# Performance work log

Measured on AMD Instinct MI355X. Metric: run time of the kernel, lower is better.

## Reference

```python
import jax, jax.numpy as jnp
import numpy as np

IN_DIM, HID, B, T = 128, 512, 32, 2048
TAU_X, TAU = 200.0, 5


def setup_inputs() -> dict:
    key = jax.random.key(0)
    ks = jax.random.split(key, 12)
    s = 0.05
    return {
        "in_seq": jax.random.normal(ks[0], (B, T, IN_DIM), jnp.float32),
        "We1": jax.random.normal(ks[1], (IN_DIM, HID), jnp.float32) * s,
        "be1": jnp.zeros((HID,), jnp.float32),
        "We2": jax.random.normal(ks[2], (HID, HID), jnp.float32) * s,
        "be2": jnp.zeros((HID,), jnp.float32),
        "We3": jax.random.normal(ks[3], (HID, HID), jnp.float32) * s,
        "be3": jnp.zeros((HID,), jnp.float32),
        # decoder: Linear+tanh, Linear+tanh
        "Wd1": jax.random.normal(ks[4], (HID, HID), jnp.float32) * s,
        "bd1": jnp.zeros((HID,), jnp.float32),
        "Wd2": jax.random.normal(ks[5], (HID, IN_DIM), jnp.float32) * s,
        "bd2": jnp.zeros((IN_DIM,), jnp.float32),
        # recurrent weight (torch: randn * 0.1)
        "W": jax.random.normal(ks[6], (HID, HID), jnp.float32) * 0.1,
    }


def reference(in_seq, We1, be1, We2, be2, We3, be3, Wd1, bd1, Wd2, bd2, W):
    def encoder(u):
        h = jnp.tanh(u @ We1 + be1)
        h = jnp.tanh(h @ We2 + be2)
        return jnp.tanh(h @ We3 + be3)

    def decoder(h):
        h = jnp.tanh(h @ Wd1 + bd1)
        return jnp.tanh(h @ Wd2 + bd2)

    x_seq = encoder(in_seq)  # [B, T, H]
    Tlen = in_seq.shape[1]
    # teacher forcing flag per step: t % tau == 0 and t > 0
    t_idx = jnp.arange(Tlen)
    tf_flags = (t_idx % TAU == 0) & (t_idx > 0)

    xs_T = jnp.swapaxes(x_seq, 0, 1)  # [T, B, H]

    def step(x, inp):
        flag, xs_t = inp
        x = jnp.where(flag, xs_t, x)
        dx = -x + jnp.tanh(x) @ W.T
        x = x + dx / TAU_X
        return x, decoder(x)  # per-step prediction [B, in_dim]

    x0 = x_seq[:, 0, :]
    _, preds = jax.lax.scan(step, x0, (tf_flags, xs_T))  # preds: [T, B, in_dim]
    x_pred = jnp.swapaxes(preds, 0, 1)  # [B, T, in_dim]
    x_recon = decoder(x_seq)  # [B, T, in_dim]
    return (x_pred, x_recon)
```

## Files before the change

### kernel.cpp

```cpp
#include <hip/hip_runtime.h>
#include <stdint.h>

#define B_SZ  32
#define T_SZ  2048
#define IN_D  128
#define HID   512
#define NCHAIN 410
#define MREC  (NCHAIN * B_SZ)
#define INV_TAUX 0.005f

typedef __attribute__((ext_vector_type(8))) short bf16x8;
typedef __attribute__((ext_vector_type(4))) float f32x4;
typedef __attribute__((ext_vector_type(4))) float float4v;
typedef __attribute__((ext_vector_type(4))) unsigned short u16x4;
typedef __attribute__((ext_vector_type(8))) unsigned short u16x8;

#define MFMA(b, a, c) __builtin_amdgcn_mfma_f32_16x16x32_bf16((b), (a), (c), 0, 0, 0)

__device__ __forceinline__ unsigned short f2bf(float x) {
  union { float f; unsigned int u; } v; v.f = x;
  unsigned int r = v.u + 0x7FFFu + ((v.u >> 16) & 1u);
  return (unsigned short)(r >> 16);
}
__device__ __forceinline__ float bf2f(unsigned short b) {
  union { unsigned int u; float f; } v; v.u = ((unsigned int)b) << 16;
  return v.f;
}
__device__ __forceinline__ float fast_tanh(float x) {
  float ax = fabsf(x);
  float e = __expf(-2.0f * ax);
  float r = (1.0f - e) * __builtin_amdgcn_rcpf(1.0f + e);
  return x < 0.0f ? -r : r;
}
__device__ __forceinline__ void gload_lds16(const void* g, void* l) {
  __builtin_amdgcn_global_load_lds(
      reinterpret_cast<__attribute__((address_space(1))) void*>(reinterpret_cast<uintptr_t>(g)),
      reinterpret_cast<__attribute__((address_space(3))) void*>(reinterpret_cast<uintptr_t>(l)),
      16, 0, 0);
}


__global__ __launch_bounds__(512) void enc_fused_k(
    const float* __restrict__ in_seq,
    const unsigned short* __restrict__ wt,
    const float* __restrict__ be1, const float* __restrict__ be2,
    const float* __restrict__ be3,
    unsigned short* __restrict__ xseq)
{
  __shared__ __attribute__((aligned(16))) unsigned short sH[64 * 512];
  unsigned short* sA = sH;

  const int tid = threadIdx.x;
  const int m0 = blockIdx.x * 64;
  const int wave = tid >> 6, lane = tid & 63;
  const int wn = wave;
  const int lrow = lane & 15, lhi = lane >> 4, sw = lrow & 7;

#pragma unroll
  for (int p = 0; p < 2; ++p) {
    int id = (p << 9) + tid;
    int row = id >> 4, cc = id & 15;
    const float* src = in_seq + (size_t)(m0 + row) * IN_D + (cc << 3);
    float4v u0 = *(const float4v*)src;
    float4v u1 = *(const float4v*)(src + 4);
    u16x8 h;
    h[0] = f2bf(u0[0]); h[1] = f2bf(u0[1]); h[2] = f2bf(u0[2]); h[3] = f2bf(u0[3]);
    h[4] = f2bf(u1[0]); h[5] = f2bf(u1[1]); h[6] = f2bf(u1[2]); h[7] = f2bf(u1[3]);
    int slot = (cc & 8) | ((cc & 7) ^ (row & 7));
    *(u16x8*)(sA + (row << 7) + (slot << 3)) = h;
  }
  __syncthreads();

  f32x4 acc[4][4];
  const unsigned short* Bts[3] = {wt, wt + 65536, wt + 327680};
  const float* bss[3] = {be1, be2, be3};

  for (int l = 0; l < 3; ++l) {
    const unsigned short* lsrc = sH;
    const int lstr = (l == 0) ? 128 : 512;
    const int nk = (l == 0) ? 4 : 16;
    const unsigned short* bl = Bts[l] + (lane << 3);
    const int nfb = (wn << 2) * nk;
    const float* bias = bss[l];

#pragma unroll
    for (int m = 0; m < 4; ++m)
#pragma unroll
      for (int n = 0; n < 4; ++n) acc[m][n] = (f32x4){0.f, 0.f, 0.f, 0.f};

    bf16x8 b0[4], b1[4];
#pragma unroll
    for (int n = 0; n < 4; ++n)
      b0[n] = *(const bf16x8*)(bl + ((nfb + n * nk) << 9));

    for (int kk = 0; kk < nk; kk += 2) {
#pragma unroll
      for (int n = 0; n < 4; ++n)
        b1[n] = *(const bf16x8*)(bl + ((nfb + n * nk + kk + 1) << 9));
      {
        const int c = (kk << 2) + lhi;
        const int slot = (c & ~7) | ((c & 7) ^ sw);
        bf16x8 af[4];
#pragma unroll
        for (int m = 0; m < 4; ++m)
          af[m] = *(const bf16x8*)(lsrc + (m * 16 + lrow) * lstr + (slot << 3));
#pragma unroll
        for (int n = 0; n < 4; ++n)
#pragma unroll
          for (int m = 0; m < 4; ++m)
            acc[m][n] = MFMA(b0[n], af[m], acc[m][n]);
      }
      if (kk + 2 < nk) {
#pragma unroll
        for (int n = 0; n < 4; ++n)
          b0[n] = *(const bf16x8*)(bl + ((nfb + n * nk + kk + 2) << 9));
      }
      {
        const int c = ((kk + 1) << 2) + lhi;
        const int slot = (c & ~7) | ((c & 7) ^ sw);
        bf16x8 af[4];
#pragma unroll
        for (int m = 0; m < 4; ++m)
          af[m] = *(const bf16x8*)(lsrc + (m * 16 + lrow) * lstr + (slot << 3));
#pragma unroll
        for (int n = 0; n < 4; ++n)
#pragma unroll
          for (int m = 0; m < 4; ++m)
            acc[m][n] = MFMA(b1[n], af[m], acc[m][n]);
      }
    }
    __syncthreads();
#pragma unroll
    for (int n = 0; n < 4; ++n) {
      const int col0 = (wn << 6) + n * 16 + (lhi << 2);
      const float4v bv = *(const float4v*)(bias + col0);
      const int c2 = col0 >> 3;
#pragma unroll
      for (int m = 0; m < 4; ++m) {
        const int row = m * 16 + lrow;
        const int slot2 = (c2 & ~7) | ((c2 & 7) ^ (row & 7));
        u16x4 h;
#pragma unroll
        for (int q = 0; q < 4; ++q) h[q] = f2bf(fast_tanh(acc[m][n][q] + bv[q]));
        *(u16x4*)(sH + (row << 9) + (slot2 << 3) + (col0 & 7)) = h;
      }
    }
    __syncthreads();
  }

#pragma unroll
  for (int p = 0; p < 8; ++p) {
    int id = (p << 9) + tid;
    int row = id >> 6, cc = id & 63;
    int slot = (cc & ~7) | ((cc & 7) ^ (row & 7));
    u16x8 v = *(const u16x8*)(sH + (row << 9) + (slot << 3));
    *(u16x8*)(xseq + ((size_t)(m0 + row) << 9) + (cc << 3)) = v;
  }
}

__global__ __launch_bounds__(512) void dec_fused_k(
    const unsigned short* __restrict__ X,
    const unsigned short* __restrict__ Wd1t,
    const unsigned short* __restrict__ Wd2t,
    const float* __restrict__ bd1, const float* __restrict__ bd2,
    float* __restrict__ out)
{
  __shared__ __attribute__((aligned(16))) unsigned short sH[64 * 512];
  unsigned short* sX = sH;

  const int tid = threadIdx.x;
  const int m0 = blockIdx.x * 64;
  const int wave = tid >> 6, lane = tid & 63;
  const int wn = wave;
  const int lrow = lane & 15, lhi = lane >> 4, sw = lrow & 7;

  char* lX = (char*)sX + tid * 16;
#pragma unroll
  for (int p = 0; p < 8; ++p) {
    int id = (p << 9) + tid;
    int row = id >> 6, cc = id & 63;
    int gcc = (cc & ~7) | ((cc & 7) ^ (row & 7));
    gload_lds16(X + ((size_t)(m0 + row) << 9) + (gcc << 3), lX + (p << 13));
  }
  __syncthreads();

  f32x4 acc[4][4];
#pragma unroll
  for (int m = 0; m < 4; ++m)
#pragma unroll
    for (int n = 0; n < 4; ++n) acc[m][n] = (f32x4){0.f, 0.f, 0.f, 0.f};

  {
    const unsigned short* bl = Wd1t + (lane << 3);
    const int nfb = (wn << 2) << 4;
    bf16x8 b0[4], b1[4];
#pragma unroll
    for (int n = 0; n < 4; ++n)
      b0[n] = *(const bf16x8*)(bl + ((nfb + (n << 4)) << 9));
    for (int kk = 0; kk < 16; kk += 2) {
#pragma unroll
      for (int n = 0; n < 4; ++n)
        b1[n] = *(const bf16x8*)(bl + ((nfb + (n << 4) + kk + 1) << 9));
      {
        const int c = (kk << 2) + lhi;
        const int slot = (c & ~7) | ((c & 7) ^ sw);
        bf16x8 af[4];
#pragma unroll
        for (int m = 0; m < 4; ++m)
          af[m] = *(const bf16x8*)(sX + ((m * 16 + lrow) << 9) + (slot << 3));
#pragma unroll
        for (int n = 0; n < 4; ++n)
#pragma unroll
          for (int m = 0; m < 4; ++m)
            acc[m][n] = MFMA(b0[n], af[m], acc[m][n]);
      }
      if (kk + 2 < 16) {
#pragma unroll
        for (int n = 0; n < 4; ++n)
          b0[n] = *(const bf16x8*)(bl + ((nfb + (n << 4) + kk + 2) << 9));
      }
      {
        const int c = ((kk + 1) << 2) + lhi;
        const int slot = (c & ~7) | ((c & 7) ^ sw);
        bf16x8 af[4];
#pragma unroll
        for (int m = 0; m < 4; ++m)
          af[m] = *(const bf16x8*)(sX + ((m * 16 + lrow) << 9) + (slot << 3));
#pragma unroll
        for (int n = 0; n < 4; ++n)
#pragma unroll
          for (int m = 0; m < 4; ++m)
            acc[m][n] = MFMA(b1[n], af[m], acc[m][n]);
      }
    }
  }
  __syncthreads();
#pragma unroll
  for (int n = 0; n < 4; ++n) {
    const int col0 = (wn << 6) + n * 16 + (lhi << 2);
    const float4v bv = *(const float4v*)(bd1 + col0);
    const int c2 = col0 >> 3;
#pragma unroll
    for (int m = 0; m < 4; ++m) {
      const int row = m * 16 + lrow;
      const int slot2 = (c2 & ~7) | ((c2 & 7) ^ (row & 7));
      u16x4 h;
#pragma unroll
      for (int q = 0; q < 4; ++q) h[q] = f2bf(fast_tanh(acc[m][n][q] + bv[q]));
      *(u16x4*)(sH + (row << 9) + (slot2 << 3) + (col0 & 7)) = h;
    }
  }
  __syncthreads();

  f32x4 acc2[4];
#pragma unroll
  for (int m = 0; m < 4; ++m) acc2[m] = (f32x4){0.f, 0.f, 0.f, 0.f};

  {
    const unsigned short* bl = Wd2t + (lane << 3);
    const int nfb = wn << 4;
    bf16x8 c0, c1;
    c0 = *(const bf16x8*)(bl + ((nfb + 0) << 9));
    for (int kk = 0; kk < 16; kk += 2) {
      c1 = *(const bf16x8*)(bl + ((nfb + kk + 1) << 9));
      {
        const int c = (kk << 2) + lhi;
        const int slot = (c & ~7) | ((c & 7) ^ sw);
#pragma unroll
        for (int m = 0; m < 4; ++m) {
          bf16x8 af = *(const bf16x8*)(sH + ((m * 16 + lrow) << 9) + (slot << 3));
          acc2[m] = MFMA(c0, af, acc2[m]);
        }
      }
      if (kk + 2 < 16)
        c0 = *(const bf16x8*)(bl + ((nfb + kk + 2) << 9));
      {
        const int c = ((kk + 1) << 2) + lhi;
        const int slot = (c & ~7) | ((c & 7) ^ sw);
#pragma unroll
        for (int m = 0; m < 4; ++m) {
          bf16x8 af = *(const bf16x8*)(sH + ((m * 16 + lrow) << 9) + (slot << 3));
          acc2[m] = MFMA(c1, af, acc2[m]);
        }
      }
    }
  }
  {
    const int col0 = (wn << 4) + (lhi << 2);
    const float4v bv = *(const float4v*)(bd2 + col0);
#pragma unroll
    for (int m = 0; m < 4; ++m) {
      const int row = m * 16 + lrow;
      float4v o;
#pragma unroll
      for (int q = 0; q < 4; ++q) o[q] = fast_tanh(acc2[m][q] + bv[q]);
      *(float4v*)(out + (size_t)(m0 + row) * IN_D + col0) = o;
    }
  }
}

__global__ __launch_bounds__(512) void rec2_k(
    const unsigned short* __restrict__ Wrec,
    const float* __restrict__ st_in,
    float* __restrict__ st_out,
    unsigned short* __restrict__ xsall,
    int s)
{
  __shared__ __attribute__((aligned(16))) unsigned short sA[32 * 512];

  const int tid = threadIdx.x;
  const int chain = blockIdx.x;
  const int wave = tid >> 6, lane = tid & 63;
  const int wn = wave;
  const int lrow = lane & 15, lhi = lane >> 4, sw = lrow & 7;
  const size_t rbase = (size_t)chain * 32;

#pragma unroll
  for (int p = 0; p < 4; ++p) {
    int id = (p << 9) + tid;
    int row = id >> 6, cc = id & 63;
    int gc = (cc & ~7) | ((cc & 7) ^ (row & 7));
    const float* src = st_in + (rbase + row) * HID + (gc << 3);
    float4v u0 = *(const float4v*)src;
    float4v u1 = *(const float4v*)(src + 4);
    u16x8 h;
    h[0] = f2bf(fast_tanh(u0[0])); h[1] = f2bf(fast_tanh(u0[1]));
    h[2] = f2bf(fast_tanh(u0[2])); h[3] = f2bf(fast_tanh(u0[3]));
    h[4] = f2bf(fast_tanh(u1[0])); h[5] = f2bf(fast_tanh(u1[1]));
    h[6] = f2bf(fast_tanh(u1[2])); h[7] = f2bf(fast_tanh(u1[3]));
    *(u16x8*)(sA + (row << 9) + (cc << 3)) = h;
  }
  __syncthreads();

  f32x4 acc[2][4];
#pragma unroll
  for (int m = 0; m < 2; ++m)
#pragma unroll
    for (int n = 0; n < 4; ++n) acc[m][n] = (f32x4){0.f, 0.f, 0.f, 0.f};

  const unsigned short* bl = Wrec + (lane << 3);
  const int nfb = (wn << 2) << 4;

  bf16x8 b0[4], b1[4];
#pragma unroll
  for (int n = 0; n < 4; ++n)
    b0[n] = *(const bf16x8*)(bl + ((nfb + (n << 4)) << 9));
  for (int kk = 0; kk < 16; kk += 2) {
#pragma unroll
    for (int n = 0; n < 4; ++n)
      b1[n] = *(const bf16x8*)(bl + ((nfb + (n << 4) + kk + 1) << 9));
    {
      const int c = (kk << 2) + lhi;
      const int slot = (c & ~7) | ((c & 7) ^ sw);
      bf16x8 af0 = *(const bf16x8*)(sA + (lrow << 9) + (slot << 3));
      bf16x8 af1 = *(const bf16x8*)(sA + ((16 + lrow) << 9) + (slot << 3));
#pragma unroll
      for (int n = 0; n < 4; ++n) {
        acc[0][n] = MFMA(b0[n], af0, acc[0][n]);
        acc[1][n] = MFMA(b0[n], af1, acc[1][n]);
      }
    }
    if (kk + 2 < 16) {
#pragma unroll
      for (int n = 0; n < 4; ++n)
        b0[n] = *(const bf16x8*)(bl + ((nfb + (n << 4) + kk + 2) << 9));
    }
    {
      const int c = ((kk + 1) << 2) + lhi;
      const int slot = (c & ~7) | ((c & 7) ^ sw);
      bf16x8 af0 = *(const bf16x8*)(sA + (lrow << 9) + (slot << 3));
      bf16x8 af1 = *(const bf16x8*)(sA + ((16 + lrow) << 9) + (slot << 3));
#pragma unroll
      for (int n = 0; n < 4; ++n) {
        acc[0][n] = MFMA(b1[n], af0, acc[0][n]);
        acc[1][n] = MFMA(b1[n], af1, acc[1][n]);
      }
    }
  }

  const int t = chain * 5 + s;
#pragma unroll
  for (int n = 0; n < 4; ++n) {
    const int col0 = (wn << 6) + n * 16 + (lhi << 2);
#pragma unroll
    for (int m = 0; m < 2; ++m) {
      const int row = m * 16 + lrow;
      const size_t gi = (rbase + row) * HID + col0;
      float4v x = *(const float4v*)(st_in + gi);
      float4v xn;
#pragma unroll
      for (int q = 0; q < 4; ++q) xn[q] = x[q] + (acc[m][n][q] - x[q]) * INV_TAUX;
      *(float4v*)(st_out + gi) = xn;
      if (t < T_SZ) {
        u16x4 h;
#pragma unroll
        for (int q = 0; q < 4; ++q) h[q] = f2bf(xn[q]);
        *(u16x4*)(xsall + ((size_t)row * T_SZ + t) * HID + col0) = h;
      }
    }
  }
}

__global__ void chain_init_k(const unsigned short* __restrict__ xseq,
                             float* __restrict__ st0) {
  int idx = blockIdx.x * blockDim.x + threadIdx.x;
  if (idx >= MREC * HID) return;
  int r = idx >> 9;
  int c = idx & 511;
  int chain = r >> 5;
  int b = r & 31;
  st0[idx] = bf2f(xseq[((size_t)b * T_SZ + chain * 5) * HID + c]);
}

__global__ void prep_k(const float* __restrict__ We1, const float* __restrict__ We2,
                       const float* __restrict__ We3, const float* __restrict__ Wd1,
                       const float* __restrict__ Wd2, const float* __restrict__ W,
                       unsigned short* __restrict__ wt) {
  int idx = blockIdx.x * blockDim.x + threadIdx.x;
  if (idx >= 1179648) return;
  unsigned short v;
  if (idx < 65536) {
    int i = idx, lane = (i >> 3) & 63, t2 = i >> 9;
    int kk = t2 & 3, nf = t2 >> 2;
    int n = (nf << 4) + (lane & 15), k = (kk << 5) + ((lane >> 4) << 3) + (i & 7);
    v = f2bf(We1[k * 512 + n]);
  } else if (idx < 327680) {
    int i = idx - 65536, lane = (i >> 3) & 63, t2 = i >> 9;
    int kk = t2 & 15, nf = t2 >> 4;
    int n = (nf << 4) + (lane & 15), k = (kk << 5) + ((lane >> 4) << 3) + (i & 7);
    v = f2bf(We2[k * 512 + n]);
  } else if (idx < 589824) {
    int i = idx - 327680, lane = (i >> 3) & 63, t2 = i >> 9;
    int kk = t2 & 15, nf = t2 >> 4;
    int n = (nf << 4) + (lane & 15), k = (kk << 5) + ((lane >> 4) << 3) + (i & 7);
    v = f2bf(We3[k * 512 + n]);
  } else if (idx < 851968) {
    int i = idx - 589824, lane = (i >> 3) & 63, t2 = i >> 9;
    int kk = t2 & 15, nf = t2 >> 4;
    int n = (nf << 4) + (lane & 15), k = (kk << 5) + ((lane >> 4) << 3) + (i & 7);
    v = f2bf(Wd1[k * 512 + n]);
  } else if (idx < 917504) {
    int i = idx - 851968, lane = (i >> 3) & 63, t2 = i >> 9;
    int kk = t2 & 15, nf = t2 >> 4;
    int n = (nf << 4) + (lane & 15), k = (kk << 5) + ((lane >> 4) << 3) + (i & 7);
    v = f2bf(Wd2[k * 128 + n]);
  } else {
    int i = idx - 917504, lane = (i >> 3) & 63, t2 = i >> 9;
    int kk = t2 & 15, nf = t2 >> 4;
    int n = (nf << 4) + (lane & 15), k = (kk << 5) + ((lane >> 4) << 3) + (i & 7);
    v = f2bf(W[(n << 9) + k]);
  }
  wt[idx] = v;
}

__global__ void sentinel_k(float* out, float v) { out[0] = v; }

extern "C" void kernel_launch(void* const* d_in, const int* in_sizes, int n_in,
                              void* d_out, int out_size, void* d_ws, size_t ws_size,
                              hipStream_t stream) {
  const float* in_seq = (const float*)d_in[0];
  const float* We1 = (const float*)d_in[1];
  const float* be1 = (const float*)d_in[2];
  const float* We2 = (const float*)d_in[3];
  const float* be2 = (const float*)d_in[4];
  const float* We3 = (const float*)d_in[5];
  const float* be3 = (const float*)d_in[6];
  const float* Wd1 = (const float*)d_in[7];
  const float* bd1 = (const float*)d_in[8];
  const float* Wd2 = (const float*)d_in[9];
  const float* bd2 = (const float*)d_in[10];
  const float* W   = (const float*)d_in[11];

  const int NROW = B_SZ * T_SZ;
  const size_t OFF_XSEQ = 0;
  const size_t OFF_WT   = (size_t)NROW * HID * 2;
  const size_t OFF_ST0  = OFF_WT + 2359296;
  const size_t OFF_ST1  = OFF_ST0 + (size_t)MREC * HID * 4;
  const size_t REQUIRED = OFF_ST1 + (size_t)MREC * HID * 4;

  float* outp = (float*)d_out;
  float* outr = outp + (size_t)NROW * IN_D;

  if (ws_size < REQUIRED) {
    sentinel_k<<<1, 1, 0, stream>>>(outp, (float)(ws_size >> 20));
    return;
  }

  char* ws = (char*)d_ws;
  unsigned short* xseq = (unsigned short*)(ws + OFF_XSEQ);
  unsigned short* wt   = (unsigned short*)(ws + OFF_WT);
  unsigned short* Wd1t = wt + 589824;
  unsigned short* Wd2t = wt + 851968;
  unsigned short* Wrec = wt + 917504;
  float* st0 = (float*)(ws + OFF_ST0);
  float* st1 = (float*)(ws + OFF_ST1);

  prep_k<<<4608, 256, 0, stream>>>(We1, We2, We3, Wd1, Wd2, W, wt);
  enc_fused_k<<<1024, 512, 0, stream>>>(in_seq, wt, be1, be2, be3, xseq);
  dec_fused_k<<<1024, 512, 0, stream>>>(xseq, Wd1t, Wd2t, bd1, bd2, outr);
  chain_init_k<<<(MREC * HID + 255) / 256, 256, 0, stream>>>(xseq, st0);
  for (int s = 0; s < 5; ++s) {
    const float* sIn  = (s & 1) ? st1 : st0;
    float*       sOut = (s & 1) ? st0 : st1;
    rec2_k<<<NCHAIN, 512, 0, stream>>>(Wrec, sIn, sOut, xseq, s);
  }
  dec_fused_k<<<1024, 512, 0, stream>>>(xseq, Wd1t, Wd2t, bd1, bd2, outp);
}
```

Before: 476.5 us.

## Fuse recon decoder into encoder and merge recurrence steps into one kernel

The encoder kernel now runs the two decoder layers directly on its LDS-resident tile, producing x_recon without re-reading x_seq from global memory. The five per-step recurrence launches and the chain-init kernel become one kernel that keeps the fp32 chain state in LDS across the five steps. This removes global state round-trips, the workspace for state buffers, and several launches. In exchange, the fused encoder kernel gets longer and the recurrence kernel uses much more LDS per block.

```diff
diff --git a/kernel.cpp b/kernel.cpp
--- a/kernel.cpp
+++ b/kernel.cpp
@@ -6,7 +6,6 @@
 #define IN_D  128
 #define HID   512
 #define NCHAIN 410
-#define MREC  (NCHAIN * B_SZ)
 #define INV_TAUX 0.005f
 
 typedef __attribute__((ext_vector_type(8))) short bf16x8;
@@ -40,12 +39,16 @@
 }
 
 
-__global__ __launch_bounds__(512) void enc_fused_k(
+__global__ __launch_bounds__(512) void enc5_k(
     const float* __restrict__ in_seq,
     const unsigned short* __restrict__ wt,
     const float* __restrict__ be1, const float* __restrict__ be2,
     const float* __restrict__ be3,
-    unsigned short* __restrict__ xseq)
+    const unsigned short* __restrict__ Wd1t,
+    const unsigned short* __restrict__ Wd2t,
+    const float* __restrict__ bd1, const float* __restrict__ bd2,
+    unsigned short* __restrict__ xseq,
+    float* __restrict__ outr)
 {
   __shared__ __attribute__((aligned(16))) unsigned short sH[64 * 512];
   unsigned short* sA = sH;
@@ -76,7 +79,6 @@
   const float* bss[3] = {be1, be2, be3};
 
   for (int l = 0; l < 3; ++l) {
-    const unsigned short* lsrc = sH;
     const int lstr = (l == 0) ? 128 : 512;
     const int nk = (l == 0) ? 4 : 16;
     const unsigned short* bl = Bts[l] + (lane << 3);
@@ -103,7 +105,7 @@
         bf16x8 af[4];
 #pragma unroll
         for (int m = 0; m < 4; ++m)
-          af[m] = *(const bf16x8*)(lsrc + (m * 16 + lrow) * lstr + (slot << 3));
+          af[m] = *(const bf16x8*)(sH + (m * 16 + lrow) * lstr + (slot << 3));
 #pragma unroll
         for (int n = 0; n < 4; ++n)
 #pragma unroll
@@ -121,7 +123,7 @@
         bf16x8 af[4];
 #pragma unroll
         for (int m = 0; m < 4; ++m)
-          af[m] = *(const bf16x8*)(lsrc + (m * 16 + lrow) * lstr + (slot << 3));
+          af[m] = *(const bf16x8*)(sH + (m * 16 + lrow) * lstr + (slot << 3));
 #pragma unroll
         for (int n = 0; n < 4; ++n)
 #pragma unroll
@@ -155,6 +157,119 @@
     int slot = (cc & ~7) | ((cc & 7) ^ (row & 7));
     u16x8 v = *(const u16x8*)(sH + (row << 9) + (slot << 3));
     *(u16x8*)(xseq + ((size_t)(m0 + row) << 9) + (cc << 3)) = v;
+  }
+
+#pragma unroll
+  for (int m = 0; m < 4; ++m)
+#pragma unroll
+    for (int n = 0; n < 4; ++n) acc[m][n] = (f32x4){0.f, 0.f, 0.f, 0.f};
+
+  {
+    const unsigned short* bl = Wd1t + (lane << 3);
+    const int nfb = (wn << 2) << 4;
+    bf16x8 b0[4], b1[4];
+#pragma unroll
+    for (int n = 0; n < 4; ++n)
+      b0[n] = *(const bf16x8*)(bl + ((nfb + (n << 4)) << 9));
+    for (int kk = 0; kk < 16; kk += 2) {
+#pragma unroll
+      for (int n = 0; n < 4; ++n)
+        b1[n] = *(const bf16x8*)(bl + ((nfb + (n << 4) + kk + 1) << 9));
+      {
+        const int c = (kk << 2) + lhi;
+        const int slot = (c & ~7) | ((c & 7) ^ sw);
+        bf16x8 af[4];
+#pragma unroll
+        for (int m = 0; m < 4; ++m)
+          af[m] = *(const bf16x8*)(sH + ((m * 16 + lrow) << 9) + (slot << 3));
+#pragma unroll
+        for (int n = 0; n < 4; ++n)
+#pragma unroll
+          for (int m = 0; m < 4; ++m)
+            acc[m][n] = MFMA(b0[n], af[m], acc[m][n]);
+      }
+      if (kk + 2 < 16) {
+#pragma unroll
+        for (int n = 0; n < 4; ++n)
+          b0[n] = *(const bf16x8*)(bl + ((nfb + (n << 4) + kk + 2) << 9));
+      }
+      {
+        const int c = ((kk + 1) << 2) + lhi;
+        const int slot = (c & ~7) | ((c & 7) ^ sw);
+        bf16x8 af[4];
+#pragma unroll
+        for (int m = 0; m < 4; ++m)
+          af[m] = *(const bf16x8*)(sH + ((m * 16 + lrow) << 9) + (slot << 3));
+#pragma unroll
+        for (int n = 0; n < 4; ++n)
+#pragma unroll
+          for (int m = 0; m < 4; ++m)
+            acc[m][n] = MFMA(b1[n], af[m], acc[m][n]);
+      }
+    }
+  }
+  __syncthreads();
+#pragma unroll
+  for (int n = 0; n < 4; ++n) {
+    const int col0 = (wn << 6) + n * 16 + (lhi << 2);
+    const float4v bv = *(const float4v*)(bd1 + col0);
+    const int c2 = col0 >> 3;
+#pragma unroll
+    for (int m = 0; m < 4; ++m) {
+      const int row = m * 16 + lrow;
+      const int slot2 = (c2 & ~7) | ((c2 & 7) ^ (row & 7));
+      u16x4 h;
+#pragma unroll
+      for (int q = 0; q < 4; ++q) h[q] = f2bf(fast_tanh(acc[m][n][q] + bv[q]));
+      *(u16x4*)(sH + (row << 9) + (slot2 << 3) + (col0 & 7)) = h;
+    }
+  }
+  __syncthreads();
+
+  f32x4 acc2[4];
+#pragma unroll
+  for (int m = 0; m < 4; ++m) acc2[m] = (f32x4){0.f, 0.f, 0.f, 0.f};
+
+  {
+    const unsigned short* bl = Wd2t + (lane << 3);
+    const int nfb = wn << 4;
+    bf16x8 c0, c1;
+    c0 = *(const bf16x8*)(bl + ((nfb + 0) << 9));
+    for (int kk = 0; kk < 16; kk += 2) {
+      c1 = *(const bf16x8*)(bl + ((nfb + kk + 1) << 9));
+      {
+        const int c = (kk << 2) + lhi;
+        const int slot = (c & ~7) | ((c & 7) ^ sw);
+#pragma unroll
+        for (int m = 0; m < 4; ++m) {
+          bf16x8 af = *(const bf16x8*)(sH + ((m * 16 + lrow) << 9) + (slot << 3));
+          acc2[m] = MFMA(c0, af, acc2[m]);
+        }
+      }
+      if (kk + 2 < 16)
+        c0 = *(const bf16x8*)(bl + ((nfb + kk + 2) << 9));
+      {
+        const int c = ((kk + 1) << 2) + lhi;
+        const int slot = (c & ~7) | ((c & 7) ^ sw);
+#pragma unroll
+        for (int m = 0; m < 4; ++m) {
+          bf16x8 af = *(const bf16x8*)(sH + ((m * 16 + lrow) << 9) + (slot << 3));
+          acc2[m] = MFMA(c1, af, acc2[m]);
+        }
+      }
+    }
+  }
+  {
+    const int col0 = (wn << 4) + (lhi << 2);
+    const float4v bv = *(const float4v*)(bd2 + col0);
+#pragma unroll
+    for (int m = 0; m < 4; ++m) {
+      const int row = m * 16 + lrow;
+      float4v o;
+#pragma unroll
+      for (int q = 0; q < 4; ++q) o[q] = fast_tanh(acc2[m][q] + bv[q]);
+      *(float4v*)(outr + (size_t)(m0 + row) * IN_D + col0) = o;
+    }
   }
 }
 
@@ -299,117 +414,117 @@
   }
 }
 
-__global__ __launch_bounds__(512) void rec2_k(
+__global__ __launch_bounds__(512) void rec_all_k(
     const unsigned short* __restrict__ Wrec,
-    const float* __restrict__ st_in,
-    float* __restrict__ st_out,
-    unsigned short* __restrict__ xsall,
-    int s)
+    unsigned short* __restrict__ xsall)
 {
+  __shared__ float xst[32][516];
   __shared__ __attribute__((aligned(16))) unsigned short sA[32 * 512];
 
   const int tid = threadIdx.x;
   const int chain = blockIdx.x;
+  const int t0 = chain * 5;
   const int wave = tid >> 6, lane = tid & 63;
   const int wn = wave;
   const int lrow = lane & 15, lhi = lane >> 4, sw = lrow & 7;
-  const size_t rbase = (size_t)chain * 32;
 
 #pragma unroll
   for (int p = 0; p < 4; ++p) {
     int id = (p << 9) + tid;
-    int row = id >> 6, cc = id & 63;
-    int gc = (cc & ~7) | ((cc & 7) ^ (row & 7));
-    const float* src = st_in + (rbase + row) * HID + (gc << 3);
-    float4v u0 = *(const float4v*)src;
-    float4v u1 = *(const float4v*)(src + 4);
-    u16x8 h;
-    h[0] = f2bf(fast_tanh(u0[0])); h[1] = f2bf(fast_tanh(u0[1]));
-    h[2] = f2bf(fast_tanh(u0[2])); h[3] = f2bf(fast_tanh(u0[3]));
-    h[4] = f2bf(fast_tanh(u1[0])); h[5] = f2bf(fast_tanh(u1[1]));
-    h[6] = f2bf(fast_tanh(u1[2])); h[7] = f2bf(fast_tanh(u1[3]));
-    *(u16x8*)(sA + (row << 9) + (cc << 3)) = h;
+    int row = id >> 6, c8 = (id & 63) << 3;
+    u16x8 v = *(const u16x8*)(xsall + (((size_t)row * T_SZ + t0) << 9) + c8);
+#pragma unroll
+    for (int e = 0; e < 8; ++e) xst[row][c8 + e] = bf2f(v[e]);
   }
   __syncthreads();
-
-  f32x4 acc[2][4];
-#pragma unroll
-  for (int m = 0; m < 2; ++m)
-#pragma unroll
-    for (int n = 0; n < 4; ++n) acc[m][n] = (f32x4){0.f, 0.f, 0.f, 0.f};
 
   const unsigned short* bl = Wrec + (lane << 3);
   const int nfb = (wn << 2) << 4;
 
-  bf16x8 b0[4], b1[4];
-#pragma unroll
-  for (int n = 0; n < 4; ++n)
-    b0[n] = *(const bf16x8*)(bl + ((nfb + (n << 4)) << 9));
-  for (int kk = 0; kk < 16; kk += 2) {
+  for (int s = 0; s < 5; ++s) {
+#pragma unroll
+    for (int p = 0; p < 4; ++p) {
+      int id = (p << 9) + tid;
+      int row = id >> 6, cc = id & 63;
+      int gc = (cc & ~7) | ((cc & 7) ^ (row & 7));
+      const float* src = &xst[row][gc << 3];
+      float4v u0 = *(const float4v*)src;
+      float4v u1 = *(const float4v*)(src + 4);
+      u16x8 h;
+      h[0] = f2bf(fast_tanh(u0[0])); h[1] = f2bf(fast_tanh(u0[1]));
+      h[2] = f2bf(fast_tanh(u0[2])); h[3] = f2bf(fast_tanh(u0[3]));
+      h[4] = f2bf(fast_tanh(u1[0])); h[5] = f2bf(fast_tanh(u1[1]));
+      h[6] = f2bf(fast_tanh(u1[2])); h[7] = f2bf(fast_tanh(u1[3]));
+      *(u16x8*)(sA + (row << 9) + (cc << 3)) = h;
+    }
+    __syncthreads();
+
+    f32x4 acc[2][4];
+#pragma unroll
+    for (int m = 0; m < 2; ++m)
+#pragma unroll
+      for (int n = 0; n < 4; ++n) acc[m][n] = (f32x4){0.f, 0.f, 0.f, 0.f};
+
+    bf16x8 b0[4], b1[4];
 #pragma unroll
     for (int n = 0; n < 4; ++n)
-      b1[n] = *(const bf16x8*)(bl + ((nfb + (n << 4) + kk + 1) << 9));
-    {
-      const int c = (kk << 2) + lhi;
-      const int slot = (c & ~7) | ((c & 7) ^ sw);
-      bf16x8 af0 = *(const bf16x8*)(sA + (lrow << 9) + (slot << 3));
-      bf16x8 af1 = *(const bf16x8*)(sA + ((16 + lrow) << 9) + (slot << 3));
-#pragma unroll
-      for (int n = 0; n < 4; ++n) {
-        acc[0][n] = MFMA(b0[n], af0, acc[0][n]);
-        acc[1][n] = MFMA(b0[n], af1, acc[1][n]);
-      }
-    }
-    if (kk + 2 < 16) {
+      b0[n] = *(const bf16x8*)(bl + ((nfb + (n << 4)) << 9));
+    for (int kk = 0; kk < 16; kk += 2) {
 #pragma unroll
       for (int n = 0; n < 4; ++n)
-        b0[n] = *(const bf16x8*)(bl + ((nfb + (n << 4) + kk + 2) << 9));
-    }
-    {
-      const int c = ((kk + 1) << 2) + lhi;
-      const int slot = (c & ~7) | ((c & 7) ^ sw);
-      bf16x8 af0 = *(const bf16x8*)(sA + (lrow << 9) + (slot << 3));
-      bf16x8 af1 = *(const bf16x8*)(sA + ((16 + lrow) << 9) + (slot << 3));
-#pragma unroll
-      for (int n = 0; n < 4; ++n) {
-        acc[0][n] = MFMA(b1[n], af0, acc[0][n]);
-        acc[1][n] = MFMA(b1[n], af1, acc[1][n]);
-      }
-    }
-  }
-
-  const int t = chain * 5 + s;
-#pragma unroll
-  for (int n = 0; n < 4; ++n) {
-    const int col0 = (wn << 6) + n * 16 + (lhi << 2);
-#pragma unroll
-    for (int m = 0; m < 2; ++m) {
-      const int row = m * 16 + lrow;
-      const size_t gi = (rbase + row) * HID + col0;
-      float4v x = *(const float4v*)(st_in + gi);
-      float4v xn;
-#pragma unroll
-      for (int q = 0; q < 4; ++q) xn[q] = x[q] + (acc[m][n][q] - x[q]) * INV_TAUX;
-      *(float4v*)(st_out + gi) = xn;
-      if (t < T_SZ) {
-        u16x4 h;
-#pragma unroll
-        for (int q = 0; q < 4; ++q) h[q] = f2bf(xn[q]);
-        *(u16x4*)(xsall + ((size_t)row * T_SZ + t) * HID + col0) = h;
-      }
-    }
-  }
-}
-
-__global__ void chain_init_k(const unsigned short* __restrict__ xseq,
-                             float* __restrict__ st0) {
-  int idx = blockIdx.x * blockDim.x + threadIdx.x;
-  if (idx >= MREC * HID) return;
-  int r = idx >> 9;
-  int c = idx & 511;
-  int chain = r >> 5;
-  int b = r & 31;
-  st0[idx] = bf2f(xseq[((size_t)b * T_SZ + chain * 5) * HID + c]);
+        b1[n] = *(const bf16x8*)(bl + ((nfb + (n << 4) + kk + 1) << 9));
+      {
+        const int c = (kk << 2) + lhi;
+        const int slot = (c & ~7) | ((c & 7) ^ sw);
+        bf16x8 af0 = *(const bf16x8*)(sA + (lrow << 9) + (slot << 3));
+        bf16x8 af1 = *(const bf16x8*)(sA + ((16 + lrow) << 9) + (slot << 3));
+#pragma unroll
+        for (int n = 0; n < 4; ++n) {
+          acc[0][n] = MFMA(b0[n], af0, acc[0][n]);
+          acc[1][n] = MFMA(b0[n], af1, acc[1][n]);
+        }
+      }
+      if (kk + 2 < 16) {
+#pragma unroll
+        for (int n = 0; n < 4; ++n)
+          b0[n] = *(const bf16x8*)(bl + ((nfb + (n << 4) + kk + 2) << 9));
+      }
+      {
+        const int c = ((kk + 1) << 2) + lhi;
+        const int slot = (c & ~7) | ((c & 7) ^ sw);
+        bf16x8 af0 = *(const bf16x8*)(sA + (lrow << 9) + (slot << 3));
+        bf16x8 af1 = *(const bf16x8*)(sA + ((16 + lrow) << 9) + (slot << 3));
+#pragma unroll
+        for (int n = 0; n < 4; ++n) {
+          acc[0][n] = MFMA(b1[n], af0, acc[0][n]);
+          acc[1][n] = MFMA(b1[n], af1, acc[1][n]);
+        }
+      }
+    }
+    __syncthreads();
+
+    const int t = t0 + s;
+#pragma unroll
+    for (int n = 0; n < 4; ++n) {
+      const int col0 = (wn << 6) + n * 16 + (lhi << 2);
+#pragma unroll
+      for (int m = 0; m < 2; ++m) {
+        const int row = m * 16 + lrow;
+        float4v x = *(const float4v*)(&xst[row][col0]);
+        float4v xn;
+#pragma unroll
+        for (int q = 0; q < 4; ++q) xn[q] = x[q] + (acc[m][n][q] - x[q]) * INV_TAUX;
+        *(float4v*)(&xst[row][col0]) = xn;
+        if (t < T_SZ) {
+          u16x4 h;
+#pragma unroll
+          for (int q = 0; q < 4; ++q) h[q] = f2bf(xn[q]);
+          *(u16x4*)(xsall + ((size_t)row * T_SZ + t) * HID + col0) = h;
+        }
+      }
+    }
+    __syncthreads();
+  }
 }
 
 __global__ void prep_k(const float* __restrict__ We1, const float* __restrict__ We2,
@@ -474,9 +589,7 @@
   const int NROW = B_SZ * T_SZ;
   const size_t OFF_XSEQ = 0;
   const size_t OFF_WT   = (size_t)NROW * HID * 2;
-  const size_t OFF_ST0  = OFF_WT + 2359296;
-  const size_t OFF_ST1  = OFF_ST0 + (size_t)MREC * HID * 4;
-  const size_t REQUIRED = OFF_ST1 + (size_t)MREC * HID * 4;
+  const size_t REQUIRED = OFF_WT + 2359296;
 
   float* outp = (float*)d_out;
   float* outr = outp + (size_t)NROW * IN_D;
@@ -492,17 +605,10 @@
   unsigned short* Wd1t = wt + 589824;
   unsigned short* Wd2t = wt + 851968;
   unsigned short* Wrec = wt + 917504;
-  float* st0 = (float*)(ws + OFF_ST0);
-  float* st1 = (float*)(ws + OFF_ST1);
 
   prep_k<<<4608, 256, 0, stream>>>(We1, We2, We3, Wd1, Wd2, W, wt);
-  enc_fused_k<<<1024, 512, 0, stream>>>(in_seq, wt, be1, be2, be3, xseq);
-  dec_fused_k<<<1024, 512, 0, stream>>>(xseq, Wd1t, Wd2t, bd1, bd2, outr);
-  chain_init_k<<<(MREC * HID + 255) / 256, 256, 0, stream>>>(xseq, st0);
-  for (int s = 0; s < 5; ++s) {
-    const float* sIn  = (s & 1) ? st1 : st0;
-    float*       sOut = (s & 1) ? st0 : st1;
-    rec2_k<<<NCHAIN, 512, 0, stream>>>(Wrec, sIn, sOut, xseq, s);
-  }
+  enc5_k<<<1024, 512, 0, stream>>>(in_seq, wt, be1, be2, be3,
+                                   Wd1t, Wd2t, bd1, bd2, xseq, outr);
+  rec_all_k<<<NCHAIN, 512, 0, stream>>>(Wrec, xseq);
   dec_fused_k<<<1024, 512, 0, stream>>>(xseq, Wd1t, Wd2t, bd1, bd2, outp);
 }
```

Result: faster. 439.7 us (-7.7%).

## Fuse encoder with recon decoder and run all recurrence steps in one kernel

Applied to the files above, without the earlier changes.

The encoder kernel now also runs the reconstruction decoder on its LDS-resident hidden tile, which removes the xseq reload and one kernel launch. The five per-step recurrence launches and the chain init kernel become a single kernel per chain that keeps the fp32 state in shared memory, eliminating the global state ping-pong buffers. The weight-load loops are also restructured into a fully unrolled four-buffer prefetch pipeline. The trade-off is higher register and LDS pressure: about 82KB of LDS in the recurrence kernel and more live B fragments.

```diff
diff --git a/kernel.cpp b/kernel.cpp
--- a/kernel.cpp
+++ b/kernel.cpp
@@ -6,7 +6,6 @@
 #define IN_D  128
 #define HID   512
 #define NCHAIN 410
-#define MREC  (NCHAIN * B_SZ)
 #define INV_TAUX 0.005f
 
 typedef __attribute__((ext_vector_type(8))) short bf16x8;
@@ -40,12 +39,93 @@
 }
 
 
-__global__ __launch_bounds__(512) void enc_fused_k(
+template<int LSTR, int MF>
+__device__ __forceinline__ void phase16(
+    const unsigned short* __restrict__ bl, int nfb,
+    const unsigned short* sbuf, int lrow, int lhi, int sw,
+    f32x4 (&acc)[MF][4])
+{
+  auto ld = [&](bf16x8 (&dst)[4], int kkv) {
+#pragma unroll
+    for (int n = 0; n < 4; ++n)
+      dst[n] = *(const bf16x8*)(bl + ((nfb + (n << 4) + kkv) << 9));
+  };
+  auto cmp = [&](bf16x8 (&buf)[4], int kkv) {
+    const int c = (kkv << 2) + lhi;
+    const int slot = (c & ~7) | ((c & 7) ^ sw);
+    bf16x8 af[MF];
+#pragma unroll
+    for (int m = 0; m < MF; ++m)
+      af[m] = *(const bf16x8*)(sbuf + (m * 16 + lrow) * LSTR + (slot << 3));
+#pragma unroll
+    for (int n = 0; n < 4; ++n)
+#pragma unroll
+      for (int m = 0; m < MF; ++m)
+        acc[m][n] = MFMA(buf[n], af[m], acc[m][n]);
+  };
+  bf16x8 bA[4], bB[4], bC[4], bD[4];
+  ld(bA, 0); ld(bB, 1); ld(bC, 2);
+  ld(bD, 3);  cmp(bA, 0);
+  ld(bA, 4);  cmp(bB, 1);
+  ld(bB, 5);  cmp(bC, 2);
+  ld(bC, 6);  cmp(bD, 3);
+  ld(bD, 7);  cmp(bA, 4);
+  ld(bA, 8);  cmp(bB, 5);
+  ld(bB, 9);  cmp(bC, 6);
+  ld(bC, 10); cmp(bD, 7);
+  ld(bD, 11); cmp(bA, 8);
+  ld(bA, 12); cmp(bB, 9);
+  ld(bB, 13); cmp(bC, 10);
+  ld(bC, 14); cmp(bD, 11);
+  ld(bD, 15); cmp(bA, 12);
+  cmp(bB, 13); cmp(bC, 14); cmp(bD, 15);
+}
+
+__device__ __forceinline__ void phase16_n1(
+    const unsigned short* __restrict__ bl, int nfb,
+    const unsigned short* sbuf, int lrow, int lhi, int sw,
+    f32x4 (&acc2)[4])
+{
+  auto ld = [&](bf16x8& dst, int kkv) {
+    dst = *(const bf16x8*)(bl + ((nfb + kkv) << 9));
+  };
+  auto cmp = [&](bf16x8& buf, int kkv) {
+    const int c = (kkv << 2) + lhi;
+    const int slot = (c & ~7) | ((c & 7) ^ sw);
+#pragma unroll
+    for (int m = 0; m < 4; ++m) {
+      bf16x8 af = *(const bf16x8*)(sbuf + ((m * 16 + lrow) << 9) + (slot << 3));
+      acc2[m] = MFMA(buf, af, acc2[m]);
+    }
+  };
+  bf16x8 c0, c1, c2, c3;
+  ld(c0, 0); ld(c1, 1); ld(c2, 2);
+  ld(c3, 3);  cmp(c0, 0);
+  ld(c0, 4);  cmp(c1, 1);
+  ld(c1, 5);  cmp(c2, 2);
+  ld(c2, 6);  cmp(c3, 3);
+  ld(c3, 7);  cmp(c0, 4);
+  ld(c0, 8);  cmp(c1, 5);
+  ld(c1, 9);  cmp(c2, 6);
+  ld(c2, 10); cmp(c3, 7);
+  ld(c3, 11); cmp(c0, 8);
+  ld(c0, 12); cmp(c1, 9);
+  ld(c1, 13); cmp(c2, 10);
+  ld(c2, 14); cmp(c3, 11);
+  ld(c3, 15); cmp(c0, 12);
+  cmp(c1, 13); cmp(c2, 14); cmp(c3, 15);
+}
+
+__global__ __launch_bounds__(512) void enc5_k(
     const float* __restrict__ in_seq,
     const unsigned short* __restrict__ wt,
     const float* __restrict__ be1, const float* __restrict__ be2,
     const float* __restrict__ be3,
-    unsigned short* __restrict__ xseq)
+    const unsigned short* __restrict__ Wd1t,
+    const unsigned short* __restrict__ Wd2t,
+    const float* __restrict__ bd1, const float* __restrict__ bd2,
+    unsigned short* __restrict__ xseq,
+    float* __restrict__ outr)
 {
   __shared__ __attribute__((aligned(16))) unsigned short sH[64 * 512];
   unsigned short* sA = sH;
@@ -72,63 +152,8 @@
   __syncthreads();
 
   f32x4 acc[4][4];
-  const unsigned short* Bts[3] = {wt, wt + 65536, wt + 327680};
-  const float* bss[3] = {be1, be2, be3};
-
-  for (int l = 0; l < 3; ++l) {
-    const unsigned short* lsrc = sH;
-    const int lstr = (l == 0) ? 128 : 512;
-    const int nk = (l == 0) ? 4 : 16;
-    const unsigned short* bl = Bts[l] + (lane << 3);
-    const int nfb = (wn << 2) * nk;
-    const float* bias = bss[l];
-
-#pragma unroll
-    for (int m = 0; m < 4; ++m)
-#pragma unroll
-      for (int n = 0; n < 4; ++n) acc[m][n] = (f32x4){0.f, 0.f, 0.f, 0.f};
-
-    bf16x8 b0[4], b1[4];
-#pragma unroll
-    for (int n = 0; n < 4; ++n)
-      b0[n] = *(const bf16x8*)(bl + ((nfb + n * nk) << 9));
-
-    for (int kk = 0; kk < nk; kk += 2) {
-#pragma unroll
-      for (int n = 0; n < 4; ++n)
-        b1[n] = *(const bf16x8*)(bl + ((nfb + n * nk + kk + 1) << 9));
-      {
-        const int c = (kk << 2) + lhi;
-        const int slot = (c & ~7) | ((c & 7) ^ sw);
-        bf16x8 af[4];
-#pragma unroll
-        for (int m = 0; m < 4; ++m)
-          af[m] = *(const bf16x8*)(lsrc + (m * 16 + lrow) * lstr + (slot << 3));
-#pragma unroll
-        for (int n = 0; n < 4; ++n)
-#pragma unroll
-          for (int m = 0; m < 4; ++m)
-            acc[m][n] = MFMA(b0[n], af[m], acc[m][n]);
-      }
-      if (kk + 2 < nk) {
-#pragma unroll
-        for (int n = 0; n < 4; ++n)
-          b0[n] = *(const bf16x8*)(bl + ((nfb + n * nk + kk + 2) << 9));
-      }
-      {
-        const int c = ((kk + 1) << 2) + lhi;
-        const int slot = (c & ~7) | ((c & 7) ^ sw);
-        bf16x8 af[4];
-#pragma unroll
-        for (int m = 0; m < 4; ++m)
-          af[m] = *(const bf16x8*)(lsrc + (m * 16 + lrow) * lstr + (slot << 3));
-#pragma unroll
-        for (int n = 0; n < 4; ++n)
-#pragma unroll
-          for (int m = 0; m < 4; ++m)
-            acc[m][n] = MFMA(b1[n], af[m], acc[m][n]);
-      }
-    }
+
+  auto epi = [&](const float* bias) {
     __syncthreads();
 #pragma unroll
     for (int n = 0; n < 4; ++n) {
@@ -146,7 +171,53 @@
       }
     }
     __syncthreads();
-  }
+  };
+
+  {
+#pragma unroll
+    for (int m = 0; m < 4; ++m)
+#pragma unroll
+      for (int n = 0; n < 4; ++n) acc[m][n] = (f32x4){0.f, 0.f, 0.f, 0.f};
+    const unsigned short* bl = wt + (lane << 3);
+    const int nfb = (wn << 2) * 4;
+    bf16x8 b0[4], b1[4], b2[4], b3[4];
+#pragma unroll
+    for (int n = 0; n < 4; ++n) {
+      b0[n] = *(const bf16x8*)(bl + ((nfb + n * 4 + 0) << 9));
+      b1[n] = *(const bf16x8*)(bl + ((nfb + n * 4 + 1) << 9));
+      b2[n] = *(const bf16x8*)(bl + ((nfb + n * 4 + 2) << 9));
+      b3[n] = *(const bf16x8*)(bl + ((nfb + n * 4 + 3) << 9));
+    }
+    auto cmp0 = [&](bf16x8 (&buf)[4], int kkv) {
+      const int c = (kkv << 2) + lhi;
+      const int slot = (c & ~7) | ((c & 7) ^ sw);
+      bf16x8 af[4];
+#pragma unroll
+      for (int m = 0; m < 4; ++m)
+        af[m] = *(const bf16x8*)(sH + (m * 16 + lrow) * 128 + (slot << 3));
+#pragma unroll
+      for (int n = 0; n < 4; ++n)
+#pragma unroll
+        for (int m = 0; m < 4; ++m)
+          acc[m][n] = MFMA(buf[n], af[m], acc[m][n]);
+    };
+    cmp0(b0, 0); cmp0(b1, 1); cmp0(b2, 2); cmp0(b3, 3);
+  }
+  epi(be1);
+
+#pragma unroll
+  for (int m = 0; m < 4; ++m)
+#pragma unroll
+    for (int n = 0; n < 4; ++n) acc[m][n] = (f32x4){0.f, 0.f, 0.f, 0.f};
+  phase16<512, 4>(wt + 65536 + (lane << 3), (wn << 2) << 4, sH, lrow, lhi, sw, acc);
+  epi(be2);
+
+#pragma unroll
+  for (int m = 0; m < 4; ++m)
+#pragma unroll
+    for (int n = 0; n < 4; ++n) acc[m][n] = (f32x4){0.f, 0.f, 0.f, 0.f};
+  phase16<512, 4>(wt + 327680 + (lane << 3), (wn << 2) << 4, sH, lrow, lhi, sw, acc);
+  epi(be3);
 
 #pragma unroll
   for (int p = 0; p < 8; ++p) {
@@ -155,6 +226,30 @@
     int slot = (cc & ~7) | ((cc & 7) ^ (row & 7));
     u16x8 v = *(const u16x8*)(sH + (row << 9) + (slot << 3));
     *(u16x8*)(xseq + ((size_t)(m0 + row) << 9) + (cc << 3)) = v;
+  }
+
+#pragma unroll
+  for (int m = 0; m < 4; ++m)
+#pragma unroll
+    for (int n = 0; n < 4; ++n) acc[m][n] = (f32x4){0.f, 0.f, 0.f, 0.f};
+  phase16<512, 4>(Wd1t + (lane << 3), (wn << 2) << 4, sH, lrow, lhi, sw, acc);
+  epi(bd1);
+
+  f32x4 acc2[4];
+#pragma unroll
+  for (int m = 0; m < 4; ++m) acc2[m] = (f32x4){0.f, 0.f, 0.f, 0.f};
+  phase16_n1(Wd2t + (lane << 3), wn << 4, sH, lrow, lhi, sw, acc2);
+  {
+    const int col0 = (wn << 4) + (lhi << 2);
+    const float4v bv = *(const float4v*)(bd2 + col0);
+#pragma unroll
+    for (int m = 0; m < 4; ++m) {
+      const int row = m * 16 + lrow;
+      float4v o;
+#pragma unroll
+      for (int q = 0; q < 4; ++q) o[q] = fast_tanh(acc2[m][q] + bv[q]);
+      *(float4v*)(outr + (size_t)(m0 + row) * IN_D + col0) = o;
+    }
   }
 }
 
@@ -189,51 +284,8 @@
   for (int m = 0; m < 4; ++m)
 #pragma unroll
     for (int n = 0; n < 4; ++n) acc[m][n] = (f32x4){0.f, 0.f, 0.f, 0.f};
-
-  {
-    const unsigned short* bl = Wd1t + (lane << 3);
-    const int nfb = (wn << 2) << 4;
-    bf16x8 b0[4], b1[4];
-#pragma unroll
-    for (int n = 0; n < 4; ++n)
-      b0[n] = *(const bf16x8*)(bl + ((nfb + (n << 4)) << 9));
-    for (int kk = 0; kk < 16; kk += 2) {
-#pragma unroll
-      for (int n = 0; n < 4; ++n)
-        b1[n] = *(const bf16x8*)(bl + ((nfb + (n << 4) + kk + 1) << 9));
-      {
-        const int c = (kk << 2) + lhi;
-        const int slot = (c & ~7) | ((c & 7) ^ sw);
-        bf16x8 af[4];
-#pragma unroll
-        for (int m = 0; m < 4; ++m)
-          af[m] = *(const bf16x8*)(sX + ((m * 16 + lrow) << 9) + (slot << 3));
-#pragma unroll
-        for (int n = 0; n < 4; ++n)
-#pragma unroll
-          for (int m = 0; m < 4; ++m)
-            acc[m][n] = MFMA(b0[n], af[m], acc[m][n]);
-      }
-      if (kk + 2 < 16) {
-#pragma unroll
-        for (int n = 0; n < 4; ++n)
-          b0[n] = *(const bf16x8*)(bl + ((nfb + (n << 4) + kk + 2) << 9));
-      }
-      {
-        const int c = ((kk + 1) << 2) + lhi;
-        const int slot = (c & ~7) | ((c & 7) ^ sw);
-        bf16x8 af[4];
-#pragma unroll
-        for (int m = 0; m < 4; ++m)
-          af[m] = *(const bf16x8*)(sX + ((m * 16 + lrow) << 9) + (slot << 3));
-#pragma unroll
-        for (int n = 0; n < 4; ++n)
-#pragma unroll
-          for (int m = 0; m < 4; ++m)
-            acc[m][n] = MFMA(b1[n], af[m], acc[m][n]);
-      }
-    }
-  }
+  phase16<512, 4>(Wd1t + (lane << 3), (wn << 2) << 4, sX, lrow, lhi, sw, acc);
+
   __syncthreads();
 #pragma unroll
   for (int n = 0; n < 4; ++n) {
@@ -255,36 +307,7 @@
   f32x4 acc2[4];
 #pragma unroll
   for (int m = 0; m < 4; ++m) acc2[m] = (f32x4){0.f, 0.f, 0.f, 0.f};
-
-  {
-    const unsigned short* bl = Wd2t + (lane << 3);
-    const int nfb = wn << 4;
-    bf16x8 c0, c1;
-    c0 = *(const bf16x8*)(bl + ((nfb + 0) << 9));
-    for (int kk = 0; kk < 16; kk += 2) {
-      c1 = *(const bf16x8*)(bl + ((nfb + kk + 1) << 9));
-      {
-        const int c = (kk << 2) + lhi;
-        const int slot = (c & ~7) | ((c & 7) ^ sw);
-#pragma unroll
-        for (int m = 0; m < 4; ++m) {
-          bf16x8 af = *(const bf16x8*)(sH + ((m * 16 + lrow) << 9) + (slot << 3));
-          acc2[m] = MFMA(c0, af, acc2[m]);
-        }
-      }
-      if (kk + 2 < 16)
-        c0 = *(const bf16x8*)(bl + ((nfb + kk + 2) << 9));
-      {
-        const int c = ((kk + 1) << 2) + lhi;
-        const int slot = (c & ~7) | ((c & 7) ^ sw);
-#pragma unroll
-        for (int m = 0; m < 4; ++m) {
-          bf16x8 af = *(const bf16x8*)(sH + ((m * 16 + lrow) << 9) + (slot << 3));
-          acc2[m] = MFMA(c1, af, acc2[m]);
-        }
-      }
-    }
-  }
+  phase16_n1(Wd2t + (lane << 3), wn << 4, sH, lrow, lhi, sw, acc2);
   {
     const int col0 = (wn << 4) + (lhi << 2);
     const float4v bv = *(const float4v*)(bd2 + col0);
@@ -299,117 +322,82 @@
   }
 }
 
-__global__ __launch_bounds__(512) void rec2_k(
+__global__ __launch_bounds__(512) void rec_all_k(
     const unsigned short* __restrict__ Wrec,
-    const float* __restrict__ st_in,
-    float* __restrict__ st_out,
-    unsigned short* __restrict__ xsall,
-    int s)
+    unsigned short* __restrict__ xsall)
 {
+  __shared__ float xst[32][516];
   __shared__ __attribute__((aligned(16))) unsigned short sA[32 * 512];
 
   const int tid = threadIdx.x;
   const int chain = blockIdx.x;
+  const int t0 = chain * 5;
   const int wave = tid >> 6, lane = tid & 63;
   const int wn = wave;
   const int lrow = lane & 15, lhi = lane >> 4, sw = lrow & 7;
-  const size_t rbase = (size_t)chain * 32;
 
 #pragma unroll
   for (int p = 0; p < 4; ++p) {
     int id = (p << 9) + tid;
-    int row = id >> 6, cc = id & 63;
-    int gc = (cc & ~7) | ((cc & 7) ^ (row & 7));
-    const float* src = st_in + (rbase + row) * HID + (gc << 3);
-    float4v u0 = *(const float4v*)src;
-    float4v u1 = *(const float4v*)(src + 4);
-    u16x8 h;
-    h[0] = f2bf(fast_tanh(u0[0])); h[1] = f2bf(fast_tanh(u0[1]));
-    h[2] = f2bf(fast_tanh(u0[2])); h[3] = f2bf(fast_tanh(u0[3]));
-    h[4] = f2bf(fast_tanh(u1[0])); h[5] = f2bf(fast_tanh(u1[1]));
-    h[6] = f2bf(fast_tanh(u1[2])); h[7] = f2bf(fast_tanh(u1[3]));
-    *(u16x8*)(sA + (row << 9) + (cc << 3)) = h;
+    int row = id >> 6, c8 = (id & 63) << 3;
+    u16x8 v = *(const u16x8*)(xsall + (((size_t)row * T_SZ + t0) << 9) + c8);
+#pragma unroll
+    for (int e = 0; e < 8; ++e) xst[row][c8 + e] = bf2f(v[e]);
   }
   __syncthreads();
-
-  f32x4 acc[2][4];
-#pragma unroll
-  for (int m = 0; m < 2; ++m)
-#pragma unroll
-    for (int n = 0; n < 4; ++n) acc[m][n] = (f32x4){0.f, 0.f, 0.f, 0.f};
 
   const unsigned short* bl = Wrec + (lane << 3);
   const int nfb = (wn << 2) << 4;
 
-  bf16x8 b0[4], b1[4];
-#pragma unroll
-  for (int n = 0; n < 4; ++n)
-    b0[n] = *(const bf16x8*)(bl + ((nfb + (n << 4)) << 9));
-  for (int kk = 0; kk < 16; kk += 2) {
-#pragma unroll
-    for (int n = 0; n < 4; ++n)
-      b1[n] = *(const bf16x8*)(bl + ((nfb + (n << 4) + kk + 1) << 9));
-    {
-      const int c = (kk << 2) + lhi;
-      const int slot = (c & ~7) | ((c & 7) ^ sw);
-      bf16x8 af0 = *(const bf16x8*)(sA + (lrow << 9) + (slot << 3));
-      bf16x8 af1 = *(const bf16x8*)(sA + ((16 + lrow) << 9) + (slot << 3));
-#pragma unroll
-      for (int n = 0; n < 4; ++n) {
-        acc[0][n] = MFMA(b0[n], af0, acc[0][n]);
-        acc[1][n] = MFMA(b0[n], af1, acc[1][n]);
+  for (int s = 0; s < 5; ++s) {
+#pragma unroll
+    for (int p = 0; p < 4; ++p) {
+      int id = (p << 9) + tid;
+      int row = id >> 6, cc = id & 63;
+      int gc = (cc & ~7) | ((cc & 7) ^ (row & 7));
+      const float* src = &xst[row][gc << 3];
+      float4v u0 = *(const float4v*)src;
+      float4v u1 = *(const float4v*)(src + 4);
+      u16x8 h;
+      h[0] = f2bf(fast_tanh(u0[0])); h[1] = f2bf(fast_tanh(u0[1]));
+      h[2] = f2bf(fast_tanh(u0[2])); h[3] = f2bf(fast_tanh(u0[3]));
+      h[4] = f2bf(fast_tanh(u1[0])); h[5] = f2bf(fast_tanh(u1[1]));
+      h[6] = f2bf(fast_tanh(u1[2])); h[7] = f2bf(fast_tanh(u1[3]));
+      *(u16x8*)(sA + (row << 9) + (cc << 3)) = h;
+    }
+    __syncthreads();
+
+    f32x4 acc[2][4];
+#pragma unroll
+    for (int m = 0; m < 2; ++m)
+#pragma unroll
+      for (int n = 0; n < 4; ++n) acc[m][n] = (f32x4){0.f, 0.f, 0.f, 0.f};
+
+    phase16<512, 2>(bl, nfb, sA, lrow, lhi, sw, acc);
+    __syncthreads();
+
+    const int t = t0 + s;
+#pragma unroll
+    for (int n = 0; n < 4; ++n) {
+      const int col0 = (wn << 6) + n * 16 + (lhi << 2);
+#pragma unroll
+      for (int m = 0; m < 2; ++m) {
+        const int row = m * 16 + lrow;
+        float4v x = *(const float4v*)(&xst[row][col0]);
+        float4v xn;
+#pragma unroll
+        for (int q = 0; q < 4; ++q) xn[q] = x[q] + (acc[m][n][q] - x[q]) * INV_TAUX;
+        *(float4v*)(&xst[row][col0]) = xn;
+        if (t < T_SZ) {
+          u16x4 h;
+#pragma unroll
+          for (int q = 0; q < 4; ++q) h[q] = f2bf(xn[q]);
+          *(u16x4*)(xsall + ((size_t)row * T_SZ + t) * HID + col0) = h;
+        }
       }
     }
-    if (kk + 2 < 16) {
-#pragma unroll
-      for (int n = 0; n < 4; ++n)
-        b0[n] = *(const bf16x8*)(bl + ((nfb + (n << 4) + kk + 2) << 9));
-    }
-    {
-      const int c = ((kk + 1) << 2) + lhi;
-      const int slot = (c & ~7) | ((c & 7) ^ sw);
-      bf16x8 af0 = *(const bf16x8*)(sA + (lrow << 9) + (slot << 3));
-      bf16x8 af1 = *(const bf16x8*)(sA + ((16 + lrow) << 9) + (slot << 3));
-#pragma unroll
-      for (int n = 0; n < 4; ++n) {
-        acc[0][n] = MFMA(b1[n], af0, acc[0][n]);
-        acc[1][n] = MFMA(b1[n], af1, acc[1][n]);
-      }
-    }
-  }
-
-  const int t = chain * 5 + s;
-#pragma unroll
-  for (int n = 0; n < 4; ++n) {
-    const int col0 = (wn << 6) + n * 16 + (lhi << 2);
-#pragma unroll
-    for (int m = 0; m < 2; ++m) {
-      const int row = m * 16 + lrow;
-      const size_t gi = (rbase + row) * HID + col0;
-      float4v x = *(const float4v*)(st_in + gi);
-      float4v xn;
-#pragma unroll
-      for (int q = 0; q < 4; ++q) xn[q] = x[q] + (acc[m][n][q] - x[q]) * INV_TAUX;
-      *(float4v*)(st_out + gi) = xn;
-      if (t < T_SZ) {
-        u16x4 h;
-#pragma unroll
-        for (int q = 0; q < 4; ++q) h[q] = f2bf(xn[q]);
-        *(u16x4*)(xsall + ((size_t)row * T_SZ + t) * HID + col0) = h;
-      }
-    }
-  }
-}
-
-__global__ void chain_init_k(const unsigned short* __restrict__ xseq,
-                             float* __restrict__ st0) {
-  int idx = blockIdx.x * blockDim.x + threadIdx.x;
-  if (idx >= MREC * HID) return;
-  int r = idx >> 9;
-  int c = idx & 511;
-  int chain = r >> 5;
-  int b = r & 31;
-  st0[idx] = bf2f(xseq[((size_t)b * T_SZ + chain * 5) * HID + c]);
+    __syncthreads();
+  }
 }
 
 __global__ void prep_k(const float* __restrict__ We1, const float* __restrict__ We2,
@@ -474,9 +462,7 @@
   const int NROW = B_SZ * T_SZ;
   const size_t OFF_XSEQ = 0;
   const size_t OFF_WT   = (size_t)NROW * HID * 2;
-  const size_t OFF_ST0  = OFF_WT + 2359296;
-  const size_t OFF_ST1  = OFF_ST0 + (size_t)MREC * HID * 4;
-  const size_t REQUIRED = OFF_ST1 + (size_t)MREC * HID * 4;
+  const size_t REQUIRED = OFF_WT + 2359296;
 
   float* outp = (float*)d_out;
   float* outr = outp + (size_t)NROW * IN_D;
@@ -492,17 +478,10 @@
   unsigned short* Wd1t = wt + 589824;
   unsigned short* Wd2t = wt + 851968;
   unsigned short* Wrec = wt + 917504;
-  float* st0 = (float*)(ws + OFF_ST0);
-  float* st1 = (float*)(ws + OFF_ST1);
 
   prep_k<<<4608, 256, 0, stream>>>(We1, We2, We3, Wd1, Wd2, W, wt);
-  enc_fused_k<<<1024, 512, 0, stream>>>(in_seq, wt, be1, be2, be3, xseq);
-  dec_fused_k<<<1024, 512, 0, stream>>>(xseq, Wd1t, Wd2t, bd1, bd2, outr);
-  chain_init_k<<<(MREC * HID + 255) / 256, 256, 0, stream>>>(xseq, st0);
-  for (int s = 0; s < 5; ++s) {
-    const float* sIn  = (s & 1) ? st1 : st0;
-    float*       sOut = (s & 1) ? st0 : st1;
-    rec2_k<<<NCHAIN, 512, 0, stream>>>(Wrec, sIn, sOut, xseq, s);
-  }
+  enc5_k<<<1024, 512, 0, stream>>>(in_seq, wt, be1, be2, be3,
+                                   Wd1t, Wd2t, bd1, bd2, xseq, outr);
+  rec_all_k<<<NCHAIN, 512, 0, stream>>>(Wrec, xseq);
   dec_fused_k<<<1024, 512, 0, stream>>>(xseq, Wd1t, Wd2t, bd1, bd2, outp);
 }
```

Result: no change. 482.1 us (+1.2%).
